# Optimization experiments

Measured on AMD Instinct MI355X. Metric: run time of the kernel, lower is better.

Reference implementation:

```python
import jax, jax.numpy as jnp
import numpy as np

T, B, I, H = 8192, 1, 1024, 1024


def _lstm_layer(x, W_ih, W_hh, b_ih, b_hh):
    # x: [T, B, I]; torch gate order: input, forget, cell(g), output
    Hh = W_hh.shape[1]
    xg = jnp.einsum('tbi,gi->tbg', x, W_ih) + b_ih + b_hh  # [T, B, 4H]

    def step(carry, xg_t):
        h, c = carry
        gates = xg_t + h @ W_hh.T  # [B, 4H]
        i, f, g, o = jnp.split(gates, 4, axis=-1)
        c = jax.nn.sigmoid(f) * c + jax.nn.sigmoid(i) * jnp.tanh(g)
        h = jax.nn.sigmoid(o) * jnp.tanh(c)
        return (h, c), h

    h0 = jnp.zeros((x.shape[1], Hh), x.dtype)
    (_, _), ys = jax.lax.scan(step, (h0, h0), xg)
    return ys  # [T, B, H]


def setup_inputs() -> dict:
    key = jax.random.key(0)
    ks = jax.random.split(key, 9)
    s = 0.02
    return {
        'inputs': jax.random.normal(ks[0], (T, B, I), dtype=jnp.float32),
        'W_ih0': jax.random.normal(ks[1], (4 * H, I), dtype=jnp.float32) * s,
        'W_hh0': jax.random.normal(ks[2], (4 * H, H), dtype=jnp.float32) * s,
        'b_ih0': jax.random.normal(ks[3], (4 * H,), dtype=jnp.float32) * s,
        'b_hh0': jax.random.normal(ks[4], (4 * H,), dtype=jnp.float32) * s,
        'W_ih1': jax.random.normal(ks[5], (4 * H, H), dtype=jnp.float32) * s,
        'W_hh1': jax.random.normal(ks[6], (4 * H, H), dtype=jnp.float32) * s,
        'b_ih1': jax.random.normal(ks[7], (4 * H,), dtype=jnp.float32) * s,
        'b_hh1': jax.random.normal(ks[8], (4 * H,), dtype=jnp.float32) * s,
    }


def reference(inputs, W_ih0, W_hh0, b_ih0, b_hh0, W_ih1, W_hh1, b_ih1, b_hh1):
    # 2-layer LSTM, zero initial state, dropout omitted (eval semantics)
    y0 = _lstm_layer(inputs, W_ih0, W_hh0, b_ih0, b_hh0)
    y1 = _lstm_layer(y0, W_ih1, W_hh1, b_ih1, b_hh1)
    return y1[-1]  # [B, H] — last timestep of top layer
```

## Files before the change

### kernel.cpp

```cpp
#include <hip/hip_runtime.h>

#define T_STEPS 8192
#define HID 1024
#define G4 4096
#define NBLK 128
#define NTHR 512
#define NSLOT 8

typedef unsigned int uint32;

struct Comm {
    uint32 hA[NSLOT][HID];
    uint32 hB[NSLOT][HID];
};

#define LD_AG  __HIP_MEMORY_SCOPE_AGENT

__device__ inline float sigm(float x) { return 1.0f / (1.0f + __expf(-x)); }
__device__ inline float tanh_f(float x) {
    x = fminf(fmaxf(x, -15.f), 15.f);
    float e = __expf(-2.0f * x);
    return (1.0f - e) / (1.0f + e);
}
__device__ inline uint32 tagf(float f, uint32 tg) {
    union { float f; uint32 u; } a; a.f = f;
    return (a.u & ~15u) | tg;
}

__global__ __launch_bounds__(256)
void gemm_xg(const float* __restrict__ A, const float* __restrict__ W,
             const float* __restrict__ bi, const float* __restrict__ bh,
             float* __restrict__ out)
{
    __shared__ float As[16][65];
    __shared__ float Bs[16][65];
    const int tid = threadIdx.x;
    const int m0 = blockIdx.y * 64, n0 = blockIdx.x * 64;
    const int tm = tid & 15, tn = tid >> 4;
    const int row = tid >> 2, q = tid & 3;
    float acc[4][4] = {{0.f}};
    for (int k0 = 0; k0 < HID; k0 += 16) {
        float4 a = *(const float4*)(A + (size_t)(m0 + row) * HID + k0 + q * 4);
        float4 b = *(const float4*)(W + (size_t)(n0 + row) * HID + k0 + q * 4);
        __syncthreads();
        As[q*4+0][row] = a.x; As[q*4+1][row] = a.y; As[q*4+2][row] = a.z; As[q*4+3][row] = a.w;
        Bs[q*4+0][row] = b.x; Bs[q*4+1][row] = b.y; Bs[q*4+2][row] = b.z; Bs[q*4+3][row] = b.w;
        __syncthreads();
#pragma unroll
        for (int kk = 0; kk < 16; ++kk) {
            float av[4], bv[4];
#pragma unroll
            for (int i = 0; i < 4; ++i) { av[i] = As[kk][tm*4+i]; bv[i] = Bs[kk][tn*4+i]; }
#pragma unroll
            for (int i = 0; i < 4; ++i)
#pragma unroll
                for (int j = 0; j < 4; ++j) acc[i][j] += av[i] * bv[j];
        }
    }
#pragma unroll
    for (int i = 0; i < 4; ++i) {
        int m = m0 + tm * 4 + i;
#pragma unroll
        for (int j = 0; j < 4; ++j) {
            int n = n0 + tn * 4 + j;
            float v = acc[i][j] + bi[n] + bh[n];
            int jd = n & (HID - 1), gate = n >> 10;
            out[(size_t)m * G4 + (jd >> 3) * 32 + (jd & 7) * 4 + gate] = v;
        }
    }
}

__device__ inline void poll8(const uint32* __restrict__ buf, uint32 tg,
                             int lane, float* __restrict__ lds)
{
    uint32 v[8];
    for (;;) {
#pragma unroll
        for (int r = 0; r < 8; ++r)
            v[r] = __hip_atomic_load(&buf[r * 64 + lane], __ATOMIC_RELAXED, LD_AG);
        bool ok = true;
#pragma unroll
        for (int r = 0; r < 8; ++r) ok &= ((v[r] & 15u) == tg);
        if (__all(ok)) break;
    }
#pragma unroll
    for (int r = 0; r < 8; ++r) {
        union { uint32 u; float f; } c; c.u = v[r];
        lds[r * 64 + lane] = c.f;
    }
}

__device__ inline void scan16(const uint32* __restrict__ buf, uint32 tg, int lane)
{
    uint32 v[16];
    for (;;) {
        bool ok = true;
#pragma unroll
        for (int r = 0; r < 16; ++r)
            v[r] = __hip_atomic_load(&buf[r * 64 + lane], __ATOMIC_RELAXED, LD_AG);
#pragma unroll
        for (int r = 0; r < 16; ++r) ok &= ((v[r] & 15u) == tg);
        if (__all(ok)) break;
    }
}

__global__ __launch_bounds__(NTHR)
void lstm_fused(const float* __restrict__ Whh0, const float* __restrict__ xg,
                const float* __restrict__ Wih1, const float* __restrict__ Whh1,
                const float* __restrict__ bih1, const float* __restrict__ bhh1,
                float* __restrict__ outF, Comm* __restrict__ cm)
{
    __shared__ float Wl[32 * HID];
    __shared__ float hlA[HID];
    __shared__ float hlB[HID];
    const int blk = blockIdx.x, tid = threadIdx.x;
    const int wave = tid >> 6, lane = tid & 63;
    const int kb = (blk < NBLK) ? blk : blk - NBLK;

    {
        const float* Wsrc = (blk < NBLK) ? Whh0 : Whh1;
#pragma unroll
        for (int i = 0; i < 16; ++i) {
            int l = i * NTHR + tid;
            int r = l >> 8, c = l & 255;
            int w = r >> 2, g = r & 3;
            ((float4*)(Wl + r * HID))[c] =
                ((const float4*)(Wsrc + (size_t)(g * HID + 8 * kb + w) * HID))[c];
        }
    }
    for (int i = tid; i < HID; i += NTHR) { hlA[i] = 0.f; hlB[i] = 0.f; }

    if (blk < NBLK) {
        const int k = kb;
        float c_state = 0.f;
        float nx0 = 0.f, nx1 = 0.f, nx2 = 0.f, nx3 = 0.f;
        if (lane == 0) {
            const float* xp = xg + k * 32 + wave * 4;
            nx0 = xp[0]; nx1 = xp[1]; nx2 = xp[2]; nx3 = xp[3];
        }
        __syncthreads();

        for (int t = 0; t < T_STEPS; ++t) {
            float x0 = nx0, x1 = nx1, x2 = nx2, x3 = nx3;
            if (lane == 0 && t + 1 < T_STEPS) {
                const float* xp = xg + (size_t)(t + 1) * G4 + k * 32 + wave * 4;
                nx0 = xp[0]; nx1 = xp[1]; nx2 = xp[2]; nx3 = xp[3];
            }
            float a0 = 0.f, a1 = 0.f, a2 = 0.f, a3 = 0.f;
            const float* wb = Wl + wave * 4 * HID;
#pragma unroll 4
            for (int u = 0; u < 16; ++u) {
                float hv = hlA[u * 64 + lane];
                a0 += wb[0 * HID + u * 64 + lane] * hv;
                a1 += wb[1 * HID + u * 64 + lane] * hv;
                a2 += wb[2 * HID + u * 64 + lane] * hv;
                a3 += wb[3 * HID + u * 64 + lane] * hv;
            }
#pragma unroll
            for (int off = 32; off > 0; off >>= 1) {
                a0 += __shfl_xor(a0, off, 64);
                a1 += __shfl_xor(a1, off, 64);
                a2 += __shfl_xor(a2, off, 64);
                a3 += __shfl_xor(a3, off, 64);
            }
            if (lane == 0) {
                float ig = sigm(x0 + a0);
                float fg = sigm(x1 + a1);
                float gg = tanh_f(x2 + a2);
                float og = sigm(x3 + a3);
                c_state = fg * c_state + ig * gg;
                float h = og * tanh_f(c_state);
                __hip_atomic_store(&cm->hA[t & 7][8 * k + wave],
                                   tagf(h, (t >> 3) & 15), __ATOMIC_RELAXED, LD_AG);
            }
            if (t == T_STEPS - 1) break;
            __syncthreads();
            if (wave == 0) {
                poll8(cm->hA[t & 7], (t >> 3) & 15, lane, hlA);
            } else if (wave == 1) {
                poll8(cm->hA[t & 7] + 512, (t >> 3) & 15, lane, hlA + 512);
            } else if (wave == 2 && t >= 4) {
                scan16(cm->hB[(t - 4) & 7], ((t - 4) >> 3) & 15, lane);
            }
            __syncthreads();
        }
    } else {
        const int j = 8 * kb + wave;
        float wreg[4][16];
#pragma unroll
        for (int g = 0; g < 4; ++g)
#pragma unroll
            for (int u = 0; u < 16; ++u)
                wreg[g][u] = Wih1[(size_t)(g * HID + j) * HID + u * 64 + lane];
        float bia[4];
#pragma unroll
        for (int g = 0; g < 4; ++g)
            bia[g] = bih1[g * HID + j] + bhh1[g * HID + j];
        float c_state = 0.f;
        __syncthreads();

        for (int t = 0; t < T_STEPS; ++t) {
            if (wave == 0) {
                poll8(cm->hA[t & 7], (t >> 3) & 15, lane, hlA);
            } else if (wave == 1) {
                poll8(cm->hA[t & 7] + 512, (t >> 3) & 15, lane, hlA + 512);
            } else if (wave == 2 && t >= 1) {
                poll8(cm->hB[(t - 1) & 7], ((t - 1) >> 3) & 15, lane, hlB);
            } else if (wave == 3 && t >= 1) {
                poll8(cm->hB[(t - 1) & 7] + 512, ((t - 1) >> 3) & 15, lane, hlB + 512);
            }
            __syncthreads();
            float a0 = 0.f, a1 = 0.f, a2 = 0.f, a3 = 0.f;
            const float* wb = Wl + wave * 4 * HID;
#pragma unroll
            for (int u = 0; u < 16; ++u) {
                float h0v = hlA[u * 64 + lane];
                float h1v = hlB[u * 64 + lane];
                a0 += wb[0 * HID + u * 64 + lane] * h1v + wreg[0][u] * h0v;
                a1 += wb[1 * HID + u * 64 + lane] * h1v + wreg[1][u] * h0v;
                a2 += wb[2 * HID + u * 64 + lane] * h1v + wreg[2][u] * h0v;
                a3 += wb[3 * HID + u * 64 + lane] * h1v + wreg[3][u] * h0v;
            }
#pragma unroll
            for (int off = 32; off > 0; off >>= 1) {
                a0 += __shfl_xor(a0, off, 64);
                a1 += __shfl_xor(a1, off, 64);
                a2 += __shfl_xor(a2, off, 64);
                a3 += __shfl_xor(a3, off, 64);
            }
            if (lane == 0) {
                float ig = sigm(bia[0] + a0);
                float fg = sigm(bia[1] + a1);
                float gg = tanh_f(bia[2] + a2);
                float og = sigm(bia[3] + a3);
                c_state = fg * c_state + ig * gg;
                float h = og * tanh_f(c_state);
                if (t == T_STEPS - 1)
                    outF[j] = h;
                else
                    __hip_atomic_store(&cm->hB[t & 7][j],
                                       tagf(h, (t >> 3) & 15), __ATOMIC_RELAXED, LD_AG);
            }
            if (t == T_STEPS - 1) break;
            __syncthreads();
        }
    }
}

extern "C" void kernel_launch(void* const* d_in, const int* in_sizes, int n_in,
                              void* d_out, int out_size, void* d_ws, size_t ws_size,
                              hipStream_t stream)
{
    const float* x    = (const float*)d_in[0];
    const float* Wih0 = (const float*)d_in[1];
    const float* Whh0 = (const float*)d_in[2];
    const float* bih0 = (const float*)d_in[3];
    const float* bhh0 = (const float*)d_in[4];
    const float* Wih1 = (const float*)d_in[5];
    const float* Whh1 = (const float*)d_in[6];
    const float* bih1 = (const float*)d_in[7];
    const float* bhh1 = (const float*)d_in[8];

    char* ws = (char*)d_ws;
    float* xg = (float*)ws;
    Comm*  cm = (Comm*)(ws + 134217728);

    (void)hipMemsetAsync(ws + 134217728, 0xFF, sizeof(Comm), stream);

    dim3 gg(G4 / 64, T_STEPS / 64);
    gemm_xg<<<gg, 256, 0, stream>>>(x, Wih0, bih0, bhh0, xg);
    lstm_fused<<<2 * NBLK, NTHR, 0, stream>>>(Whh0, xg, Wih1, Whh1, bih1, bhh1,
                                              (float*)d_out, cm);
}
```

Measured before the change: 36.22 ms.

## Merge both LSTM layers into one wavefront-pipelined block with register-resident weights

Instead of separate block groups for layer 0 and layer 1, each of 128 blocks now computes both layers, with layer 1 lagging one step behind layer 0. All three recurrent and input weight slices are held in registers rather than LDS. The h vectors are double-buffered in LDS so only one barrier per step is needed. Polling uses vectorized dwordx4 system-coherent loads with per-chunk completion tracking and a short sleep. This is meant to cut the number of grid-wide handoffs and barriers per step, at the cost of heavy register pressure (192 weight floats per thread) and serializing both layers' work within a block.

```diff
diff --git a/kernel.cpp b/kernel.cpp
--- a/kernel.cpp
+++ b/kernel.cpp
@@ -70,38 +70,46 @@
     }
 }
 
-__device__ inline void poll8(const uint32* __restrict__ buf, uint32 tg,
-                             int lane, float* __restrict__ lds)
-{
-    uint32 v[8];
+__device__ __forceinline__ void red4(float& a0, float& a1, float& a2, float& a3)
+{
+#pragma unroll
+    for (int off = 32; off > 0; off >>= 1) {
+        a0 += __shfl_xor(a0, off, 64);
+        a1 += __shfl_xor(a1, off, 64);
+        a2 += __shfl_xor(a2, off, 64);
+        a3 += __shfl_xor(a3, off, 64);
+    }
+}
+
+__device__ __forceinline__ void poll_gather(const uint32* __restrict__ buf, uint32 tg,
+                                            int lane, float* __restrict__ lds)
+{
+    const uint32* p = buf + lane * 4;
+    uint4 v0, v1, v2, v3;
+    unsigned done = 0;
     for (;;) {
-#pragma unroll
-        for (int r = 0; r < 8; ++r)
-            v[r] = __hip_atomic_load(&buf[r * 64 + lane], __ATOMIC_RELAXED, LD_AG);
-        bool ok = true;
-#pragma unroll
-        for (int r = 0; r < 8; ++r) ok &= ((v[r] & 15u) == tg);
-        if (__all(ok)) break;
-    }
-#pragma unroll
-    for (int r = 0; r < 8; ++r) {
-        union { uint32 u; float f; } c; c.u = v[r];
-        lds[r * 64 + lane] = c.f;
-    }
-}
-
-__device__ inline void scan16(const uint32* __restrict__ buf, uint32 tg, int lane)
-{
-    uint32 v[16];
-    for (;;) {
-        bool ok = true;
-#pragma unroll
-        for (int r = 0; r < 16; ++r)
-            v[r] = __hip_atomic_load(&buf[r * 64 + lane], __ATOMIC_RELAXED, LD_AG);
-#pragma unroll
-        for (int r = 0; r < 16; ++r) ok &= ((v[r] & 15u) == tg);
-        if (__all(ok)) break;
-    }
+        if (!(done & 1u)) asm volatile("global_load_dwordx4 %0, %1, off sc0 sc1"             : "=v"(v0) : "v"(p) : "memory");
+        if (!(done & 2u)) asm volatile("global_load_dwordx4 %0, %1, off offset:1024 sc0 sc1" : "=v"(v1) : "v"(p) : "memory");
+        if (!(done & 4u)) asm volatile("global_load_dwordx4 %0, %1, off offset:2048 sc0 sc1" : "=v"(v2) : "v"(p) : "memory");
+        if (!(done & 8u)) asm volatile("global_load_dwordx4 %0, %1, off offset:3072 sc0 sc1" : "=v"(v3) : "v"(p) : "memory");
+        asm volatile("s_waitcnt vmcnt(0)" ::: "memory");
+        __builtin_amdgcn_sched_barrier(0);
+        if (!(done & 1u) && (v0.x & 15u) == tg && (v0.y & 15u) == tg &&
+            (v0.z & 15u) == tg && (v0.w & 15u) == tg) done |= 1u;
+        if (!(done & 2u) && (v1.x & 15u) == tg && (v1.y & 15u) == tg &&
+            (v1.z & 15u) == tg && (v1.w & 15u) == tg) done |= 2u;
+        if (!(done & 4u) && (v2.x & 15u) == tg && (v2.y & 15u) == tg &&
+            (v2.z & 15u) == tg && (v2.w & 15u) == tg) done |= 4u;
+        if (!(done & 8u) && (v3.x & 15u) == tg && (v3.y & 15u) == tg &&
+            (v3.z & 15u) == tg && (v3.w & 15u) == tg) done |= 8u;
+        if (__all(done == 15u)) break;
+        __builtin_amdgcn_s_sleep(1);
+    }
+    union { uint4 u; float4 f; } c;
+    c.u = v0; ((float4*)lds)[  0 + lane] = c.f;
+    c.u = v1; ((float4*)lds)[ 64 + lane] = c.f;
+    c.u = v2; ((float4*)lds)[128 + lane] = c.f;
+    c.u = v3; ((float4*)lds)[192 + lane] = c.f;
 }
 
 __global__ __launch_bounds__(NTHR)
@@ -110,139 +118,117 @@
                 const float* __restrict__ bih1, const float* __restrict__ bhh1,
                 float* __restrict__ outF, Comm* __restrict__ cm)
 {
-    __shared__ float Wl[32 * HID];
-    __shared__ float hlA[HID];
-    __shared__ float hlB[HID];
-    const int blk = blockIdx.x, tid = threadIdx.x;
+    __shared__ float hlA[2][HID];
+    __shared__ float hlB[2][HID];
+    const int tid = threadIdx.x;
     const int wave = tid >> 6, lane = tid & 63;
-    const int kb = (blk < NBLK) ? blk : blk - NBLK;
-
+    const int kb = blockIdx.x;
+    const int j = 8 * kb + wave;
+
+    float whh0[4][16], whh1[4][16], wih1[4][16];
+#pragma unroll
+    for (int g = 0; g < 4; ++g) {
+        const float* p0 = Whh0 + (size_t)(g * HID + j) * HID + lane;
+        const float* p1 = Whh1 + (size_t)(g * HID + j) * HID + lane;
+        const float* p2 = Wih1 + (size_t)(g * HID + j) * HID + lane;
+#pragma unroll
+        for (int u = 0; u < 16; ++u) {
+            whh0[g][u] = p0[u * 64];
+            whh1[g][u] = p1[u * 64];
+            wih1[g][u] = p2[u * 64];
+        }
+    }
+    float bia[4];
+#pragma unroll
+    for (int g = 0; g < 4; ++g) bia[g] = bih1[g * HID + j] + bhh1[g * HID + j];
+
+    for (int i = tid; i < HID; i += NTHR) {
+        hlA[0][i] = 0.f; hlA[1][i] = 0.f; hlB[0][i] = 0.f; hlB[1][i] = 0.f;
+    }
+
+    float c0 = 0.f, c1 = 0.f;
+    float nx0 = 0.f, nx1 = 0.f, nx2 = 0.f, nx3 = 0.f;
+    if (lane == 0) {
+        const float* xp = xg + kb * 32 + wave * 4;
+        nx0 = xp[0]; nx1 = xp[1]; nx2 = xp[2]; nx3 = xp[3];
+    }
+    __syncthreads();
+
+    for (int t = 0; t < T_STEPS; ++t) {
+        const int p = t & 1;
+        const float* hA = hlA[p];
+        const float* hB = hlB[p];
+        float x0 = nx0, x1 = nx1, x2 = nx2, x3 = nx3;
+        if (lane == 0 && t + 1 < T_STEPS) {
+            const float* xp = xg + (size_t)(t + 1) * G4 + kb * 32 + wave * 4;
+            nx0 = xp[0]; nx1 = xp[1]; nx2 = xp[2]; nx3 = xp[3];
+        }
+        float a0 = 0.f, a1 = 0.f, a2 = 0.f, a3 = 0.f;
+#pragma unroll
+        for (int u = 0; u < 16; ++u) {
+            float hv = hA[u * 64 + lane];
+            a0 += whh0[0][u] * hv; a1 += whh0[1][u] * hv;
+            a2 += whh0[2][u] * hv; a3 += whh0[3][u] * hv;
+        }
+        red4(a0, a1, a2, a3);
+        if (lane == 0) {
+            float ig = sigm(x0 + a0), fg = sigm(x1 + a1);
+            float gg = tanh_f(x2 + a2), og = sigm(x3 + a3);
+            c0 = fg * c0 + ig * gg;
+            float h = og * tanh_f(c0);
+            __hip_atomic_store(&cm->hA[t & 7][j], tagf(h, (t >> 3) & 15),
+                               __ATOMIC_RELAXED, LD_AG);
+        }
+        if (t >= 1) {
+            float b0 = 0.f, b1 = 0.f, b2 = 0.f, b3 = 0.f;
+#pragma unroll
+            for (int u = 0; u < 16; ++u) {
+                float h0v = hA[u * 64 + lane];
+                float h1v = hB[u * 64 + lane];
+                b0 += whh1[0][u] * h1v + wih1[0][u] * h0v;
+                b1 += whh1[1][u] * h1v + wih1[1][u] * h0v;
+                b2 += whh1[2][u] * h1v + wih1[2][u] * h0v;
+                b3 += whh1[3][u] * h1v + wih1[3][u] * h0v;
+            }
+            red4(b0, b1, b2, b3);
+            if (lane == 0) {
+                float ig = sigm(bia[0] + b0), fg = sigm(bia[1] + b1);
+                float gg = tanh_f(bia[2] + b2), og = sigm(bia[3] + b3);
+                c1 = fg * c1 + ig * gg;
+                float h = og * tanh_f(c1);
+                __hip_atomic_store(&cm->hB[(t - 1) & 7][j],
+                                   tagf(h, ((t - 1) >> 3) & 15),
+                                   __ATOMIC_RELAXED, LD_AG);
+            }
+        }
+        if (wave == 0) {
+            poll_gather((const uint32*)cm->hA[t & 7], (uint32)((t >> 3) & 15),
+                        lane, hlA[p ^ 1]);
+        } else if (wave == 1 && t >= 1) {
+            poll_gather((const uint32*)cm->hB[(t - 1) & 7],
+                        (uint32)(((t - 1) >> 3) & 15), lane, hlB[p ^ 1]);
+        }
+        __syncthreads();
+    }
     {
-        const float* Wsrc = (blk < NBLK) ? Whh0 : Whh1;
-#pragma unroll
-        for (int i = 0; i < 16; ++i) {
-            int l = i * NTHR + tid;
-            int r = l >> 8, c = l & 255;
-            int w = r >> 2, g = r & 3;
-            ((float4*)(Wl + r * HID))[c] =
-                ((const float4*)(Wsrc + (size_t)(g * HID + 8 * kb + w) * HID))[c];
-        }
-    }
-    for (int i = tid; i < HID; i += NTHR) { hlA[i] = 0.f; hlB[i] = 0.f; }
-
-    if (blk < NBLK) {
-        const int k = kb;
-        float c_state = 0.f;
-        float nx0 = 0.f, nx1 = 0.f, nx2 = 0.f, nx3 = 0.f;
+        const float* hA = hlA[T_STEPS & 1];
+        const float* hB = hlB[T_STEPS & 1];
+        float b0 = 0.f, b1 = 0.f, b2 = 0.f, b3 = 0.f;
+#pragma unroll
+        for (int u = 0; u < 16; ++u) {
+            float h0v = hA[u * 64 + lane];
+            float h1v = hB[u * 64 + lane];
+            b0 += whh1[0][u] * h1v + wih1[0][u] * h0v;
+            b1 += whh1[1][u] * h1v + wih1[1][u] * h0v;
+            b2 += whh1[2][u] * h1v + wih1[2][u] * h0v;
+            b3 += whh1[3][u] * h1v + wih1[3][u] * h0v;
+        }
+        red4(b0, b1, b2, b3);
         if (lane == 0) {
-            const float* xp = xg + k * 32 + wave * 4;
-            nx0 = xp[0]; nx1 = xp[1]; nx2 = xp[2]; nx3 = xp[3];
-        }
-        __syncthreads();
-
-        for (int t = 0; t < T_STEPS; ++t) {
-            float x0 = nx0, x1 = nx1, x2 = nx2, x3 = nx3;
-            if (lane == 0 && t + 1 < T_STEPS) {
-                const float* xp = xg + (size_t)(t + 1) * G4 + k * 32 + wave * 4;
-                nx0 = xp[0]; nx1 = xp[1]; nx2 = xp[2]; nx3 = xp[3];
-            }
-            float a0 = 0.f, a1 = 0.f, a2 = 0.f, a3 = 0.f;
-            const float* wb = Wl + wave * 4 * HID;
-#pragma unroll 4
-            for (int u = 0; u < 16; ++u) {
-                float hv = hlA[u * 64 + lane];
-                a0 += wb[0 * HID + u * 64 + lane] * hv;
-                a1 += wb[1 * HID + u * 64 + lane] * hv;
-                a2 += wb[2 * HID + u * 64 + lane] * hv;
-                a3 += wb[3 * HID + u * 64 + lane] * hv;
-            }
-#pragma unroll
-            for (int off = 32; off > 0; off >>= 1) {
-                a0 += __shfl_xor(a0, off, 64);
-                a1 += __shfl_xor(a1, off, 64);
-                a2 += __shfl_xor(a2, off, 64);
-                a3 += __shfl_xor(a3, off, 64);
-            }
-            if (lane == 0) {
-                float ig = sigm(x0 + a0);
-                float fg = sigm(x1 + a1);
-                float gg = tanh_f(x2 + a2);
-                float og = sigm(x3 + a3);
-                c_state = fg * c_state + ig * gg;
-                float h = og * tanh_f(c_state);
-                __hip_atomic_store(&cm->hA[t & 7][8 * k + wave],
-                                   tagf(h, (t >> 3) & 15), __ATOMIC_RELAXED, LD_AG);
-            }
-            if (t == T_STEPS - 1) break;
-            __syncthreads();
-            if (wave == 0) {
-                poll8(cm->hA[t & 7], (t >> 3) & 15, lane, hlA);
-            } else if (wave == 1) {
-                poll8(cm->hA[t & 7] + 512, (t >> 3) & 15, lane, hlA + 512);
-            } else if (wave == 2 && t >= 4) {
-                scan16(cm->hB[(t - 4) & 7], ((t - 4) >> 3) & 15, lane);
-            }
-            __syncthreads();
-        }
-    } else {
-        const int j = 8 * kb + wave;
-        float wreg[4][16];
-#pragma unroll
-        for (int g = 0; g < 4; ++g)
-#pragma unroll
-            for (int u = 0; u < 16; ++u)
-                wreg[g][u] = Wih1[(size_t)(g * HID + j) * HID + u * 64 + lane];
-        float bia[4];
-#pragma unroll
-        for (int g = 0; g < 4; ++g)
-            bia[g] = bih1[g * HID + j] + bhh1[g * HID + j];
-        float c_state = 0.f;
-        __syncthreads();
-
-        for (int t = 0; t < T_STEPS; ++t) {
-            if (wave == 0) {
-                poll8(cm->hA[t & 7], (t >> 3) & 15, lane, hlA);
-            } else if (wave == 1) {
-                poll8(cm->hA[t & 7] + 512, (t >> 3) & 15, lane, hlA + 512);
-            } else if (wave == 2 && t >= 1) {
-                poll8(cm->hB[(t - 1) & 7], ((t - 1) >> 3) & 15, lane, hlB);
-            } else if (wave == 3 && t >= 1) {
-                poll8(cm->hB[(t - 1) & 7] + 512, ((t - 1) >> 3) & 15, lane, hlB + 512);
-            }
-            __syncthreads();
-            float a0 = 0.f, a1 = 0.f, a2 = 0.f, a3 = 0.f;
-            const float* wb = Wl + wave * 4 * HID;
-#pragma unroll
-            for (int u = 0; u < 16; ++u) {
-                float h0v = hlA[u * 64 + lane];
-                float h1v = hlB[u * 64 + lane];
-                a0 += wb[0 * HID + u * 64 + lane] * h1v + wreg[0][u] * h0v;
-                a1 += wb[1 * HID + u * 64 + lane] * h1v + wreg[1][u] * h0v;
-                a2 += wb[2 * HID + u * 64 + lane] * h1v + wreg[2][u] * h0v;
-                a3 += wb[3 * HID + u * 64 + lane] * h1v + wreg[3][u] * h0v;
-            }
-#pragma unroll
-            for (int off = 32; off > 0; off >>= 1) {
-                a0 += __shfl_xor(a0, off, 64);
-                a1 += __shfl_xor(a1, off, 64);
-                a2 += __shfl_xor(a2, off, 64);
-                a3 += __shfl_xor(a3, off, 64);
-            }
-            if (lane == 0) {
-                float ig = sigm(bia[0] + a0);
-                float fg = sigm(bia[1] + a1);
-                float gg = tanh_f(bia[2] + a2);
-                float og = sigm(bia[3] + a3);
-                c_state = fg * c_state + ig * gg;
-                float h = og * tanh_f(c_state);
-                if (t == T_STEPS - 1)
-                    outF[j] = h;
-                else
-                    __hip_atomic_store(&cm->hB[t & 7][j],
-                                       tagf(h, (t >> 3) & 15), __ATOMIC_RELAXED, LD_AG);
-            }
-            if (t == T_STEPS - 1) break;
-            __syncthreads();
+            float ig = sigm(bia[0] + b0), fg = sigm(bia[1] + b1);
+            float gg = tanh_f(bia[2] + b2), og = sigm(bia[3] + b3);
+            c1 = fg * c1 + ig * gg;
+            outF[j] = og * tanh_f(c1);
         }
     }
 }
@@ -269,6 +255,6 @@
 
     dim3 gg(G4 / 64, T_STEPS / 64);
     gemm_xg<<<gg, 256, 0, stream>>>(x, Wih0, bih0, bhh0, xg);
-    lstm_fused<<<2 * NBLK, NTHR, 0, stream>>>(Whh0, xg, Wih1, Whh1, bih1, bhh1,
-                                              (float*)d_out, cm);
-}
+    lstm_fused<<<NBLK, NTHR, 0, stream>>>(Whh0, xg, Wih1, Whh1, bih1, bhh1,
+                                          (float*)d_out, cm);
+}
```

Result: slower. 42.40 ms (+17.1%).
